# Optimization experiments

Hardware: AMD Instinct MI355X
Metric: run time of the kernel (lower is better)

Reference implementation:

```python
import jax, jax.numpy as jnp
import numpy as np

OUTPUT_SIZES = [1, 3, 6, 8]  # SPP pyramid -> total KV length 110

def _bounds(n, out):
    # PyTorch AdaptiveMaxPool2d bin boundaries
    return [((i * n) // out, -((-(i + 1) * n) // out)) for i in range(out)]

def adaptive_max_pool2d(x, out):
    # x: [B, C, H, W] -> [B, C, out, out]
    B, C, H, W = x.shape
    rows = jnp.stack([x[:, :, s:e, :].max(axis=2) for s, e in _bounds(H, out)], axis=2)
    return jnp.stack([rows[:, :, :, s:e].max(axis=3) for s, e in _bounds(W, out)], axis=3)

def spp(x):
    # [B, C, H, W] -> [B, C, S] with S = sum(o*o) = 110
    B, C = x.shape[:2]
    return jnp.concatenate(
        [adaptive_max_pool2d(x, o).reshape(B, C, o * o) for o in OUTPUT_SIZES], axis=2)

def conv1x1(x, w):
    # 1x1 conv, no bias: w [O, C], x [B, C, H, W]
    return jnp.einsum('oc,bchw->bohw', w, x)

def setup_inputs() -> dict:
    key = jax.random.key(0)
    ks = jax.random.split(key, 6)
    B, C, H, W = 16, 512, 64, 64
    IC = C // 2
    x = jax.random.normal(ks[0], (B, C, H, W), jnp.float32)
    y = jax.random.normal(ks[1], (B, C, H, W), jnp.float32)
    sc = 1.0 / np.sqrt(C)
    w_phi = jax.random.normal(ks[2], (IC, C), jnp.float32) * sc
    w_theta = jax.random.normal(ks[3], (IC, C), jnp.float32) * sc
    w_g = jax.random.normal(ks[4], (IC, C), jnp.float32) * sc
    w_mask = jax.random.normal(ks[5], (C, IC), jnp.float32) * (1.0 / np.sqrt(IC))
    return {"x": x, "y": y, "w_phi": w_phi, "w_theta": w_theta,
            "w_g": w_g, "w_mask": w_mask}

def reference(x, y, w_phi, w_theta, w_g, w_mask):
    B, C, H, W = x.shape
    IC = w_phi.shape[0]
    N = H * W
    # Query: [B, N, IC]
    x_phi = conv1x1(x, w_phi).reshape(B, IC, N).transpose(0, 2, 1)
    # Keys/values from SPP-pooled y: [B, IC, S] / [B, S, IC]
    y_theta = spp(conv1x1(y, w_theta))
    y_g = spp(conv1x1(y, w_g)).transpose(0, 2, 1)
    # Attention with softmax over the QUERY axis (dim=1), as in the source
    attn = jax.nn.softmax(jnp.einsum('bnc,bcs->bns', x_phi, y_theta), axis=1)
    agg = jnp.einsum('bns,bsc->bnc', attn, y_g)          # [B, N, IC]
    agg = agg.transpose(0, 2, 1).reshape(B, IC, H, W)     # [B, IC, H, W]
    mask = conv1x1(agg, w_mask)                           # [B, C, H, W]
    return mask + x
```

## Files before the change

### kernel.cpp

```cpp
#include <hip/hip_runtime.h>

#define DI __device__ __forceinline__

typedef __attribute__((ext_vector_type(8))) __bf16 bf16x8;
typedef __attribute__((ext_vector_type(4))) float f32x4;

DI unsigned short f2bf(float x) {
  union { float f; unsigned u; } v; v.f = x;
  unsigned r = v.u + 0x7fffu + ((v.u >> 16) & 1u);
  return (unsigned short)(r >> 16);
}
DI float bf2f(unsigned short h) {
  union { unsigned u; float f; } v; v.u = ((unsigned)h) << 16;
  return v.f;
}
DI unsigned pack2(float a, float b) {
  return (unsigned)f2bf(a) | (((unsigned)f2bf(b)) << 16);
}

DI void gl_lds16(const void* g, void* l) {
  __builtin_amdgcn_global_load_lds(
      (const __attribute__((address_space(1))) void*)g,
      (__attribute__((address_space(3))) void*)l, 16, 0, 0);
}

__global__ __launch_bounds__(256) void pw_conv(
    const float* __restrict__ w_theta, const float* __restrict__ w_g,
    unsigned short* __restrict__ wTG)
{
  int e = (blockIdx.x * 256 + threadIdx.x) * 8;
  const float* src = (e < 131072) ? (w_theta + e) : (w_g + (e - 131072));
  float4 a = *(const float4*)src;
  float4 c = *(const float4*)(src + 4);
  uint4 u;
  u.x = pack2(a.x, a.y); u.y = pack2(a.z, a.w);
  u.z = pack2(c.x, c.y); u.w = pack2(c.z, c.w);
  *(uint4*)(wTG + e) = u;
}

__constant__ int c_RS[18] = {0, 0,21,42, 0,10,21,32,42,53, 0,8,16,24,32,40,48,56};
__constant__ int c_RE[18] = {64, 22,43,64, 11,22,32,43,54,64, 8,16,24,32,40,48,56,64};

__global__ __launch_bounds__(256) void k1f_conv_pool(
    const float* __restrict__ y, const unsigned short* __restrict__ wTG,
    unsigned short* __restrict__ Rbuf)
{
  const int tid = threadIdx.x;
  const int id = blockIdx.x;
  const int tile = (id & 7) * 16 + (id >> 3);
  const int mb = (tile & 3) * 128;
  const int nbt = tile >> 2;
  const int nb = nbt * 128;
  const int b  = blockIdx.y;
  const int lane = tid & 63, wv = tid >> 6;
  const int wm = (wv & 1) * 64, wn = (wv >> 1) * 64;
  const int l15 = lane & 15, l4 = lane >> 4;

  __shared__ __align__(16) char smem[2 * 18432];
  float* P = (float*)smem;

  const int xn = tid & 127, xh = tid >> 7;
  const float* ycol = y + ((size_t)(b * 512 + xh * 16)) * 4096 + nb + xn;

  f32x4 acc[4][4];
  #pragma unroll
  for (int i = 0; i < 4; ++i)
    #pragma unroll
    for (int j = 0; j < 4; ++j) acc[i][j] = f32x4{0.f, 0.f, 0.f, 0.f};

  float xrA[16], xrB[16];
  auto yload = [&](float* xr, int kb) {
    const float* p = ycol + (size_t)kb * 4096;
    #pragma unroll
    for (int k = 0; k < 16; ++k) xr[k] = p[(size_t)k * 4096];
  };
  auto dmaA = [&](int buf, int kb) {
    unsigned short* As = (unsigned short*)(smem + buf * 18432);
    #pragma unroll
    for (int p = 0; p < 2; ++p) {
      int chunk = (wv * 2 + p) * 64 + lane;
      int row = chunk >> 2, c16 = chunk & 3;
      gl_lds16(wTG + ((size_t)(mb + row)) * 512 + kb + c16 * 8,
               As + (wv * 2 + p) * 512);
    }
  };
  auto bwrite = [&](int buf, const float* xr) {
    unsigned short* Bs = (unsigned short*)(smem + buf * 18432 + 8192);
    unsigned u[8];
    #pragma unroll
    for (int k = 0; k < 16; k += 2) u[k >> 1] = pack2(xr[k], xr[k + 1]);
    uint4* d = (uint4*)&Bs[xn * 40 + xh * 16];
    d[0] = make_uint4(u[0], u[1], u[2], u[3]);
    d[1] = make_uint4(u[4], u[5], u[6], u[7]);
  };
  auto mfma_step = [&](int buf) {
    const unsigned short* As = (const unsigned short*)(smem + buf * 18432);
    const unsigned short* Bs = As + 4096;
    bf16x8 af[4], bfr[4];
    #pragma unroll
    for (int i = 0; i < 4; ++i)
      af[i] = *(const bf16x8*)&As[(wm + i * 16 + l15) * 32 + l4 * 8];
    #pragma unroll
    for (int j = 0; j < 4; ++j)
      bfr[j] = *(const bf16x8*)&Bs[(wn + j * 16 + l15) * 40 + l4 * 8];
    #pragma unroll
    for (int i = 0; i < 4; ++i)
      #pragma unroll
      for (int j = 0; j < 4; ++j)
        acc[i][j] = __builtin_amdgcn_mfma_f32_16x16x32_bf16(af[i], bfr[j], acc[i][j], 0, 0, 0);
  };

  yload(xrA, 0);
  dmaA(0, 0);
  bwrite(0, xrA);
  yload(xrB, 32);
  __syncthreads();
  for (int t = 0; t < 16; t += 2) {
    dmaA(1, (t + 1) * 32);
    bwrite(1, xrB);
    if (t + 2 < 16) yload(xrA, (t + 2) * 32);
    mfma_step(0);
    __syncthreads();
    if (t + 2 < 16) { dmaA(0, (t + 2) * 32); bwrite(0, xrA); }
    if (t + 3 < 16) yload(xrB, (t + 3) * 32);
    mfma_step(1);
    __syncthreads();
  }

  const int hloc = wv >> 1;
  #pragma unroll
  for (int pass = 0; pass < 2; ++pass) {
    __syncthreads();
    if (hloc == pass) {
      #pragma unroll
      for (int i = 0; i < 4; ++i)
        #pragma unroll
        for (int j = 0; j < 4; ++j)
          #pragma unroll
          for (int r = 0; r < 4; ++r)
            P[(wm + i * 16 + l4 * 4 + r) * 65 + j * 16 + l15] = acc[i][j][r];
    }
    __syncthreads();
    const int o = tid & 127;
    size_t rbase = (((size_t)(b * 64 + nbt * 2 + pass)) * 18) * 512 + mb + o;
    if (tid < 128) {
      float b0 = -3.4e38f, b1 = b0, b2 = b0, b3 = b0;
      #pragma unroll
      for (int w = 0; w < 64; ++w) {
        float v = P[o * 65 + w];
        b0 = fmaxf(b0, v);
        if (w < 22) b1 = fmaxf(b1, v);
        if (w >= 21 && w < 43) b2 = fmaxf(b2, v);
        if (w >= 42) b3 = fmaxf(b3, v);
      }
      Rbuf[rbase]           = f2bf(b0);
      Rbuf[rbase + 512]     = f2bf(b1);
      Rbuf[rbase + 2 * 512] = f2bf(b2);
      Rbuf[rbase + 3 * 512] = f2bf(b3);
    } else {
      float s6[6], s8[8];
      #pragma unroll
      for (int i = 0; i < 6; ++i) s6[i] = -3.4e38f;
      #pragma unroll
      for (int i = 0; i < 8; ++i) s8[i] = -3.4e38f;
      constexpr int R6S[6] = {0, 10, 21, 32, 42, 53};
      constexpr int R6E[6] = {11, 22, 32, 43, 54, 64};
      #pragma unroll
      for (int w = 0; w < 64; ++w) {
        float v = P[o * 65 + w];
        #pragma unroll
        for (int i = 0; i < 6; ++i)
          if (w >= R6S[i] && w < R6E[i]) s6[i] = fmaxf(s6[i], v);
        s8[w >> 3] = fmaxf(s8[w >> 3], v);
      }
      #pragma unroll
      for (int i = 0; i < 6; ++i) Rbuf[rbase + (size_t)(4 + i) * 512] = f2bf(s6[i]);
      #pragma unroll
      for (int i = 0; i < 8; ++i) Rbuf[rbase + (size_t)(10 + i) * 512] = f2bf(s8[i]);
    }
  }
}

__global__ __launch_bounds__(256) void k2_pool_final(
    const unsigned short* __restrict__ Rbuf, float* __restrict__ Pt,
    float* __restrict__ Pg)
{
  const int s = blockIdx.x, b = blockIdx.y, tid = threadIdx.x;
  size_t obase = ((size_t)(b * 128) + s) * 256 + tid;
  if (s >= 110) { Pt[obase] = 0.f; Pg[obase] = 0.f; return; }
  int he, wb;
  if (s == 0)      { he = 0; wb = 0; }
  else if (s < 10) { int i = s - 1;  he = 1 + i / 3;  wb = 1 + i % 3; }
  else if (s < 46) { int i = s - 10; he = 4 + i / 6;  wb = 4 + i % 6; }
  else             { int i = s - 46; he = 10 + i / 8; wb = 10 + i % 8; }
  float m0 = -3.4e38f, m1 = -3.4e38f;
  int e = c_RE[he];
  for (int h = c_RS[he]; h < e; ++h) {
    const unsigned short* r = Rbuf + (((size_t)(b * 64 + h)) * 18 + wb) * 512;
    m0 = fmaxf(m0, bf2f(r[tid]));
    m1 = fmaxf(m1, bf2f(r[tid + 256]));
  }
  Pt[obase] = m0;
  Pg[obase] = m1;
}

__global__ __launch_bounds__(256) void k3_fused(
    const float* __restrict__ Pt, const float* __restrict__ Pg,
    const float* __restrict__ w_phi, const float* __restrict__ w_mask,
    unsigned short* __restrict__ Kth, unsigned short* __restrict__ Ktl,
    unsigned short* __restrict__ Vb)
{
  __shared__ __align__(16) char sm3[51200];
  const int tid = threadIdx.x;
  const int tx = tid & 15, ty = tid >> 4;
  const int b = blockIdx.y;
  if (blockIdx.z == 0) {
    const int ct = blockIdx.x;
    const int c0 = tx * 4, s0 = ty * 8;
    float* Ls = (float*)sm3;
    float* Ws = Ls + 128 * 64;
    float acc[8][4] = {};
    for (int kc = 0; kc < 256; kc += 64) {
      #pragma unroll
      for (int j = 0; j < 8; ++j) {
        int flat = tid + 256 * j;
        int row = flat >> 4, k4 = (flat & 15) << 2;
        *(float4*)&Ls[row * 64 + k4] =
            *(const float4*)(Pt + ((size_t)(b * 128) + row) * 256 + kc + k4);
      }
      #pragma unroll
      for (int j = 0; j < 4; ++j) {
        int flat = tid + 256 * j;
        int row = flat >> 4, c4 = (flat & 15) << 2;
        *(float4*)&Ws[row * 68 + c4] =
            *(const float4*)(w_phi + (size_t)(kc + row) * 512 + ct * 64 + c4);
      }
      __syncthreads();
      for (int k = 0; k < 64; k += 4) {
        float4 wv[4];
        #pragma unroll
        for (int kk = 0; kk < 4; ++kk) wv[kk] = *(const float4*)&Ws[(k + kk) * 68 + c0];
        #pragma unroll
        for (int i = 0; i < 8; ++i) {
          float4 a = *(const float4*)&Ls[(s0 + i) * 64 + k];
          const float* ap = (const float*)&a;
          #pragma unroll
          for (int kk = 0; kk < 4; ++kk) {
            const float* wp = (const float*)&wv[kk];
            acc[i][0] += ap[kk] * wp[0];
            acc[i][1] += ap[kk] * wp[1];
            acc[i][2] += ap[kk] * wp[2];
            acc[i][3] += ap[kk] * wp[3];
          }
        }
      }
      __syncthreads();
    }
    #pragma unroll
    for (int i = 0; i < 8; ++i) {
      unsigned short hi[4]; float lo[4];
      #pragma unroll
      for (int j = 0; j < 4; ++j) { hi[j] = f2bf(acc[i][j]); lo[j] = acc[i][j] - bf2f(hi[j]); }
      size_t base = ((size_t)(b * 128) + s0 + i) * 512 + ct * 64 + c0;
      uint2 uh; uh.x = (unsigned)hi[0] | ((unsigned)hi[1] << 16);
      uh.y = (unsigned)hi[2] | ((unsigned)hi[3] << 16);
      uint2 ul; ul.x = pack2(lo[0], lo[1]); ul.y = pack2(lo[2], lo[3]);
      *(uint2*)&Kth[base] = uh;
      *(uint2*)&Ktl[base] = ul;
    }
  } else {
    const int ot = blockIdx.x;
    const int o0 = ty * 4;
    float* Ws = (float*)sm3;
    float* Ps = Ws + 64 * 64;
    float acc[4][8] = {};
    for (int kc = 0; kc < 256; kc += 64) {
      #pragma unroll
      for (int j = 0; j < 4; ++j) {
        int flat = tid + 256 * j;
        int row = flat >> 4, k4 = (flat & 15) << 2;
        *(float4*)&Ws[row * 64 + k4] =
            *(const float4*)(w_mask + (size_t)(ot * 64 + row) * 256 + kc + k4);
      }
      #pragma unroll
      for (int j = 0; j < 8; ++j) {
        int flat = tid + 256 * j;
        int row = flat >> 4, k4 = (flat & 15) << 2;
        *(float4*)&Ps[row * 68 + k4] =
            *(const float4*)(Pg + ((size_t)(b * 128) + row) * 256 + kc + k4);
      }
      __syncthreads();
      for (int k = 0; k < 64; k += 4) {
        float4 wv[4];
        #pragma unroll
        for (int i = 0; i < 4; ++i) wv[i] = *(const float4*)&Ws[(o0 + i) * 64 + k];
        #pragma unroll
        for (int jj = 0; jj < 8; ++jj) {
          float4 pv = *(const float4*)&Ps[(tx + 16 * jj) * 68 + k];
          const float* pp = (const float*)&pv;
          #pragma unroll
          for (int i = 0; i < 4; ++i) {
            const float* wp = (const float*)&wv[i];
            #pragma unroll
            for (int kk = 0; kk < 4; ++kk) acc[i][jj] += wp[kk] * pp[kk];
          }
        }
      }
      __syncthreads();
    }
    #pragma unroll
    for (int i = 0; i < 4; ++i)
      #pragma unroll
      for (int jj = 0; jj < 8; ++jj)
        Vb[((size_t)(b * 512) + ot * 64 + o0 + i) * 128 + tx + 16 * jj] =
            f2bf(acc[i][jj]);
  }
}

__global__ __launch_bounds__(256) void k4_scores(
    const float* __restrict__ x, const unsigned short* __restrict__ Kth,
    const unsigned short* __restrict__ Ktl, float* __restrict__ scoresT,
    float* __restrict__ pmax_g, float* __restrict__ psum_g)
{
  const int tid = threadIdx.x;
  const int ntile = blockIdx.x;
  const int nb = ntile * 128;
  const int b = blockIdx.y;
  const int lane = tid & 63, wv = tid >> 6;
  const int wm = (wv & 1) * 64, wn = (wv >> 1) * 64;
  const int l15 = lane & 15, l4 = lane >> 4;
  __shared__ __align__(16) char smem4[2 * 26624];
  __shared__ float SmP[256], SsP[256];

  const int xn = tid & 127, xh = tid >> 7;
  const float* xcol = x + ((size_t)(b * 512 + xh * 16)) * 4096 + nb + xn;

  f32x4 acc[4][4];
  #pragma unroll
  for (int i = 0; i < 4; ++i)
    #pragma unroll
    for (int j = 0; j < 4; ++j) acc[i][j] = f32x4{0.f, 0.f, 0.f, 0.f};

  float xrA[16], xrB[16];
  auto xload = [&](float* xr, int kb) {
    const float* p = xcol + (size_t)kb * 4096;
    #pragma unroll
    for (int k = 0; k < 16; ++k) xr[k] = p[(size_t)k * 4096];
  };
  auto dmaA = [&](int buf, int kb) {
    unsigned short* Ah = (unsigned short*)(smem4 + buf * 26624);
    unsigned short* Al = Ah + 4096;
    #pragma unroll
    for (int p = 0; p < 2; ++p) {
      int chunk = (wv * 2 + p) * 64 + lane;
      int row = chunk >> 2, c16 = chunk & 3;
      size_t g = ((size_t)(b * 128) + row) * 512 + kb + c16 * 8;
      gl_lds16(Kth + g, Ah + (wv * 2 + p) * 512);
      gl_lds16(Ktl + g, Al + (wv * 2 + p) * 512);
    }
  };
  auto bwrite = [&](int buf, const float* xr) {
    unsigned short* Bs = (unsigned short*)(smem4 + buf * 26624 + 16384);
    unsigned u[8];
    #pragma unroll
    for (int k = 0; k < 16; k += 2) u[k >> 1] = pack2(xr[k], xr[k + 1]);
    uint4* d = (uint4*)&Bs[xn * 40 + xh * 16];
    d[0] = make_uint4(u[0], u[1], u[2], u[3]);
    d[1] = make_uint4(u[4], u[5], u[6], u[7]);
  };
  auto mfma_step = [&](int buf) {
    const unsigned short* Ah = (const unsigned short*)(smem4 + buf * 26624);
    const unsigned short* Al = Ah + 4096;
    const unsigned short* Bs = Al + 4096;
    bf16x8 ah[4], al[4], bfr[4];
    #pragma unroll
    for (int i = 0; i < 4; ++i) {
      ah[i] = *(const bf16x8*)&Ah[(wm + i * 16 + l15) * 32 + l4 * 8];
      al[i] = *(const bf16x8*)&Al[(wm + i * 16 + l15) * 32 + l4 * 8];
    }
    #pragma unroll
    for (int j = 0; j < 4; ++j)
      bfr[j] = *(const bf16x8*)&Bs[(wn + j * 16 + l15) * 40 + l4 * 8];
    #pragma unroll
    for (int i = 0; i < 4; ++i)
      #pragma unroll
      for (int j = 0; j < 4; ++j) {
        acc[i][j] = __builtin_amdgcn_mfma_f32_16x16x32_bf16(ah[i], bfr[j], acc[i][j], 0, 0, 0);
        acc[i][j] = __builtin_amdgcn_mfma_f32_16x16x32_bf16(al[i], bfr[j], acc[i][j], 0, 0, 0);
      }
  };

  xload(xrA, 0);
  dmaA(0, 0);
  bwrite(0, xrA);
  xload(xrB, 32);
  __syncthreads();
  for (int t = 0; t < 16; t += 2) {
    dmaA(1, (t + 1) * 32);
    bwrite(1, xrB);
    if (t + 2 < 16) xload(xrA, (t + 2) * 32);
    mfma_step(0);
    __syncthreads();
    if (t + 2 < 16) { dmaA(0, (t + 2) * 32); bwrite(0, xrA); }
    if (t + 3 < 16) xload(xrB, (t + 3) * 32);
    mfma_step(1);
    __syncthreads();
  }

  #pragma unroll
  for (int i = 0; i < 4; ++i)
    #pragma unroll
    for (int j = 0; j < 4; ++j)
      *(float4*)(scoresT + ((size_t)(b * 4096) + nb + wn + j * 16 + l15) * 128 +
                 wm + i * 16 + l4 * 4) = *(float4*)&acc[i][j];

  const int nh = wn >> 6;
  float cm[4][4];
  #pragma unroll
  for (int i = 0; i < 4; ++i)
    #pragma unroll
    for (int r = 0; r < 4; ++r) {
      float v = fmaxf(fmaxf(acc[i][0][r], acc[i][1][r]),
                      fmaxf(acc[i][2][r], acc[i][3][r]));
      v = fmaxf(v, __shfl_xor(v, 1));
      v = fmaxf(v, __shfl_xor(v, 2));
      v = fmaxf(v, __shfl_xor(v, 4));
      v = fmaxf(v, __shfl_xor(v, 8));
      if (l15 == 0) SmP[(wm + i * 16 + l4 * 4 + r) * 2 + nh] = v;
    }
  __syncthreads();
  #pragma unroll
  for (int i = 0; i < 4; ++i)
    #pragma unroll
    for (int r = 0; r < 4; ++r) {
      int s = wm + i * 16 + l4 * 4 + r;
      cm[i][r] = fmaxf(SmP[s * 2], SmP[s * 2 + 1]);
    }
  #pragma unroll
  for (int i = 0; i < 4; ++i)
    #pragma unroll
    for (int r = 0; r < 4; ++r) {
      float s0 = __expf(acc[i][0][r] - cm[i][r]) + __expf(acc[i][1][r] - cm[i][r]) +
                 __expf(acc[i][2][r] - cm[i][r]) + __expf(acc[i][3][r] - cm[i][r]);
      s0 += __shfl_xor(s0, 1);
      s0 += __shfl_xor(s0, 2);
      s0 += __shfl_xor(s0, 4);
      s0 += __shfl_xor(s0, 8);
      if (l15 == 0) SsP[(wm + i * 16 + l4 * 4 + r) * 2 + nh] = s0;
    }
  __syncthreads();
  if (tid < 128) {
    size_t pidx = ((size_t)(b * 128) + tid) * 32 + ntile;
    pmax_g[pidx] = fmaxf(SmP[tid * 2], SmP[tid * 2 + 1]);
    psum_g[pidx] = SsP[tid * 2] + SsP[tid * 2 + 1];
  }
}

__global__ __launch_bounds__(256) void k5e_exp(
    const float* __restrict__ scoresT, const float* __restrict__ pmax_g,
    const float* __restrict__ psum_g, unsigned short* __restrict__ Eb)
{
  const int b = blockIdx.y, tid = threadIdx.x;
  __shared__ float sm[128], sl[128];
  if (tid < 128) {
    float M = 0.f, linv = 0.f;
    if (tid < 110) {
      const float* pm = pmax_g + ((size_t)(b * 128) + tid) * 32;
      const float* ps = psum_g + ((size_t)(b * 128) + tid) * 32;
      M = -3.4e38f;
      #pragma unroll
      for (int t = 0; t < 32; ++t) M = fmaxf(M, pm[t]);
      float S = 0.f;
      #pragma unroll
      for (int t = 0; t < 32; ++t) S += ps[t] * __expf(pm[t] - M);
      linv = 1.f / S;
    }
    sm[tid] = M; sl[tid] = linv;
  }
  __syncthreads();
  const size_t base = (size_t)b * 4096 * 128;
  #pragma unroll
  for (int j = 0; j < 8; ++j) {
    int chunk = blockIdx.x * 2048 + j * 256 + tid;
    int sc = (chunk & 31) * 4;
    float4 v = *(const float4*)(scoresT + base + (size_t)chunk * 4);
    float e0 = __expf(v.x - sm[sc])     * sl[sc];
    float e1 = __expf(v.y - sm[sc + 1]) * sl[sc + 1];
    float e2 = __expf(v.z - sm[sc + 2]) * sl[sc + 2];
    float e3 = __expf(v.w - sm[sc + 3]) * sl[sc + 3];
    uint2 u; u.x = pack2(e0, e1); u.y = pack2(e2, e3);
    *(uint2*)(Eb + base + (size_t)chunk * 4) = u;
  }
}

__global__ __launch_bounds__(256) void k6_out(
    const unsigned short* __restrict__ Eb, const unsigned short* __restrict__ Vb,
    const float* __restrict__ x, float* __restrict__ out)
{
  const int tid = threadIdx.x;
  const int id = blockIdx.x;
  const int tile = (id & 7) * 16 + (id >> 3);
  const int mb = (tile & 3) * 128;
  const int nb = (tile >> 2) * 128;
  const int b = blockIdx.y;
  const int lane = tid & 63, wv = tid >> 6;
  const int wm = (wv & 1) * 64, wn = (wv >> 1) * 64;
  const int l15 = lane & 15, l4 = lane >> 4;
  __shared__ __align__(16) unsigned short SA[4][4096];
  __shared__ __align__(16) unsigned short SB[4][4096];

  #pragma unroll
  for (int h = 0; h < 4; ++h)
    #pragma unroll
    for (int p = 0; p < 2; ++p) {
      int chunk = (wv * 2 + p) * 64 + lane;
      int row = chunk >> 2, c16 = chunk & 3;
      gl_lds16(Vb + ((size_t)(b * 512) + mb + row) * 128 + h * 32 + c16 * 8,
               &SA[h][(wv * 2 + p) * 512]);
      gl_lds16(Eb + ((size_t)(b * 4096) + nb + row) * 128 + h * 32 + c16 * 8,
               &SB[h][(wv * 2 + p) * 512]);
    }

  float xr[4][4][4];
  #pragma unroll
  for (int i = 0; i < 4; ++i)
    #pragma unroll
    for (int j = 0; j < 4; ++j)
      #pragma unroll
      for (int r = 0; r < 4; ++r)
        xr[i][j][r] = x[((size_t)(b * 512) + mb + wm + i * 16 + l4 * 4 + r) * 4096 +
                        nb + wn + j * 16 + l15];

  f32x4 acc[4][4];
  #pragma unroll
  for (int i = 0; i < 4; ++i)
    #pragma unroll
    for (int j = 0; j < 4; ++j) acc[i][j] = f32x4{0.f, 0.f, 0.f, 0.f};

  __syncthreads();
  #pragma unroll
  for (int h = 0; h < 4; ++h) {
    bf16x8 af[4], bfr[4];
    #pragma unroll
    for (int i = 0; i < 4; ++i)
      af[i] = *(const bf16x8*)&SA[h][(wm + i * 16 + l15) * 32 + l4 * 8];
    #pragma unroll
    for (int j = 0; j < 4; ++j)
      bfr[j] = *(const bf16x8*)&SB[h][(wn + j * 16 + l15) * 32 + l4 * 8];
    #pragma unroll
    for (int i = 0; i < 4; ++i)
      #pragma unroll
      for (int j = 0; j < 4; ++j)
        acc[i][j] = __builtin_amdgcn_mfma_f32_16x16x32_bf16(af[i], bfr[j], acc[i][j], 0, 0, 0);
  }
  #pragma unroll
  for (int i = 0; i < 4; ++i)
    #pragma unroll
    for (int j = 0; j < 4; ++j)
      #pragma unroll
      for (int r = 0; r < 4; ++r) {
        int o = mb + wm + i * 16 + l4 * 4 + r;
        size_t idx = ((size_t)(b * 512) + o) * 4096 + nb + wn + j * 16 + l15;
        out[idx] = acc[i][j][r] + xr[i][j][r];
      }
}

extern "C" void kernel_launch(void* const* d_in, const int* in_sizes, int n_in,
                              void* d_out, int out_size, void* d_ws, size_t ws_size,
                              hipStream_t stream)
{
  (void)in_sizes; (void)n_in; (void)out_size; (void)ws_size;
  const float* x       = (const float*)d_in[0];
  const float* y       = (const float*)d_in[1];
  const float* w_phi   = (const float*)d_in[2];
  const float* w_theta = (const float*)d_in[3];
  const float* w_g     = (const float*)d_in[4];
  const float* w_mask  = (const float*)d_in[5];
  float* out = (float*)d_out;

  char* ws = (char*)d_ws;
  char* B0 = ws + 67108864;
  unsigned short* Rbuf = (unsigned short*)B0;
  float* scoresT = (float*)B0;
  unsigned short* Eb = (unsigned short*)(B0 + 33554432);
  unsigned short* wTG = (unsigned short*)(B0 + 50331648);
  unsigned short* Vb  = (unsigned short*)(B0 + 50331648);
  float* pmax_g = (float*)(B0 + 52428800);
  float* psum_g = (float*)(B0 + 52690944);
  char* C0 = B0 + 54525952;
  float* Pt = (float*)C0;
  float* Pg = (float*)(C0 + 2097152);
  unsigned short* Kth = (unsigned short*)(C0 + 4194304);
  unsigned short* Ktl = (unsigned short*)(C0 + 6291456);

  pw_conv<<<dim3(128), 256, 0, stream>>>(w_theta, w_g, wTG);
  k1f_conv_pool<<<dim3(128, 16), 256, 0, stream>>>(y, wTG, Rbuf);
  k2_pool_final<<<dim3(128, 16), 256, 0, stream>>>(Rbuf, Pt, Pg);
  k3_fused<<<dim3(8, 16, 2), 256, 0, stream>>>(Pt, Pg, w_phi, w_mask, Kth, Ktl, Vb);
  k4_scores<<<dim3(32, 16), 256, 0, stream>>>(x, Kth, Ktl, scoresT, pmax_g, psum_g);
  k5e_exp<<<dim3(64, 16), 256, 0, stream>>>(scoresT, pmax_g, psum_g, Eb);
  k6_out<<<dim3(128, 16), 256, 0, stream>>>(Eb, Vb, x, out);
}
```

Baseline: 487.4 us.

## Triple-buffer GEMM mainloops with explicit vmcnt waits and vectorized activation loads

In the conv+pool and scores kernels, the main loops move from a double-buffered schedule with two __syncthreads per pair of steps to a triple-buffered LDS ring. Each step now has a single s_barrier gated by hand-counted s_waitcnt vmcnt values, so async DMA and activation loads stay in flight across MFMA steps. Activation loads switch from 16 scalar strided loads per thread to four float4 loads, each thread now covering 4 positions by 4 channels. The B-tile LDS writes are reshaped to match. This raises LDS use, which may lower occupancy, and the hardcoded vmcnt counts are fragile if the compiler reorders or splits memory operations.

```diff
diff --git a/kernel.cpp b/kernel.cpp
--- a/kernel.cpp
+++ b/kernel.cpp
@@ -23,6 +23,12 @@
       (const __attribute__((address_space(1))) void*)g,
       (__attribute__((address_space(3))) void*)l, 16, 0, 0);
 }
+
+DI void wt_vm0()  { asm volatile("s_waitcnt vmcnt(0) lgkmcnt(0)" ::: "memory"); }
+DI void wt_vm6()  { asm volatile("s_waitcnt vmcnt(6) lgkmcnt(0)" ::: "memory"); }
+DI void wt_vm8()  { asm volatile("s_waitcnt vmcnt(8) lgkmcnt(0)" ::: "memory"); }
+DI void wt_vm10() { asm volatile("s_waitcnt vmcnt(10) lgkmcnt(0)" ::: "memory"); }
+DI void wt_vm12() { asm volatile("s_waitcnt vmcnt(12) lgkmcnt(0)" ::: "memory"); }
 
 __global__ __launch_bounds__(256) void pw_conv(
     const float* __restrict__ w_theta, const float* __restrict__ w_g,
@@ -56,11 +62,11 @@
   const int wm = (wv & 1) * 64, wn = (wv >> 1) * 64;
   const int l15 = lane & 15, l4 = lane >> 4;
 
-  __shared__ __align__(16) char smem[2 * 18432];
+  __shared__ __align__(16) char smem[3 * 18432];
   float* P = (float*)smem;
 
-  const int xn = tid & 127, xh = tid >> 7;
-  const float* ycol = y + ((size_t)(b * 512 + xh * 16)) * 4096 + nb + xn;
+  const int c4 = tid & 7, n4 = tid >> 3;
+  const float* ycol = y + ((size_t)(b * 512)) * 4096 + nb + n4 * 4;
 
   f32x4 acc[4][4];
   #pragma unroll
@@ -68,30 +74,32 @@
     #pragma unroll
     for (int j = 0; j < 4; ++j) acc[i][j] = f32x4{0.f, 0.f, 0.f, 0.f};
 
-  float xrA[16], xrB[16];
+  float xr0[16], xr1[16];
   auto yload = [&](float* xr, int kb) {
-    const float* p = ycol + (size_t)kb * 4096;
-    #pragma unroll
-    for (int k = 0; k < 16; ++k) xr[k] = p[(size_t)k * 4096];
+    #pragma unroll
+    for (int cc = 0; cc < 4; ++cc)
+      *(float4*)&xr[cc * 4] =
+          *(const float4*)(ycol + (size_t)(kb + c4 * 4 + cc) * 4096);
   };
   auto dmaA = [&](int buf, int kb) {
     unsigned short* As = (unsigned short*)(smem + buf * 18432);
     #pragma unroll
     for (int p = 0; p < 2; ++p) {
       int chunk = (wv * 2 + p) * 64 + lane;
-      int row = chunk >> 2, c16 = chunk & 3;
-      gl_lds16(wTG + ((size_t)(mb + row)) * 512 + kb + c16 * 8,
+      int row = chunk >> 2, cc16 = chunk & 3;
+      gl_lds16(wTG + ((size_t)(mb + row)) * 512 + kb + cc16 * 8,
                As + (wv * 2 + p) * 512);
     }
   };
   auto bwrite = [&](int buf, const float* xr) {
     unsigned short* Bs = (unsigned short*)(smem + buf * 18432 + 8192);
-    unsigned u[8];
-    #pragma unroll
-    for (int k = 0; k < 16; k += 2) u[k >> 1] = pack2(xr[k], xr[k + 1]);
-    uint4* d = (uint4*)&Bs[xn * 40 + xh * 16];
-    d[0] = make_uint4(u[0], u[1], u[2], u[3]);
-    d[1] = make_uint4(u[4], u[5], u[6], u[7]);
+    #pragma unroll
+    for (int q = 0; q < 4; ++q) {
+      uint2 u;
+      u.x = pack2(xr[q], xr[4 + q]);
+      u.y = pack2(xr[8 + q], xr[12 + q]);
+      *(uint2*)&Bs[(n4 * 4 + q) * 40 + c4 * 4] = u;
+    }
   };
   auto mfma_step = [&](int buf) {
     const unsigned short* As = (const unsigned short*)(smem + buf * 18432);
@@ -110,21 +118,21 @@
         acc[i][j] = __builtin_amdgcn_mfma_f32_16x16x32_bf16(af[i], bfr[j], acc[i][j], 0, 0, 0);
   };
 
-  yload(xrA, 0);
+  yload(xr0, 0);
   dmaA(0, 0);
-  bwrite(0, xrA);
-  yload(xrB, 32);
-  __syncthreads();
-  for (int t = 0; t < 16; t += 2) {
-    dmaA(1, (t + 1) * 32);
-    bwrite(1, xrB);
-    if (t + 2 < 16) yload(xrA, (t + 2) * 32);
-    mfma_step(0);
-    __syncthreads();
-    if (t + 2 < 16) { dmaA(0, (t + 2) * 32); bwrite(0, xrA); }
-    if (t + 3 < 16) yload(xrB, (t + 3) * 32);
-    mfma_step(1);
-    __syncthreads();
+  bwrite(0, xr0);
+  yload(xr1, 32);
+  #pragma unroll
+  for (int t = 0; t < 16; ++t) {
+    if (t + 1 < 16) dmaA((t + 1) % 3, (t + 1) * 32);
+    if (t + 2 < 16) yload((t & 1) ? xr1 : xr0, (t + 2) * 32);
+    if (t < 14) wt_vm10();
+    else if (t == 14) wt_vm6();
+    else wt_vm0();
+    __builtin_amdgcn_s_barrier();
+    __builtin_amdgcn_sched_barrier(0);
+    mfma_step(t % 3);
+    if (t + 1 < 16) bwrite((t + 1) % 3, (t & 1) ? xr0 : xr1);
   }
 
   const int hloc = wv >> 1;
@@ -231,9 +239,9 @@
       #pragma unroll
       for (int j = 0; j < 4; ++j) {
         int flat = tid + 256 * j;
-        int row = flat >> 4, c4 = (flat & 15) << 2;
-        *(float4*)&Ws[row * 68 + c4] =
-            *(const float4*)(w_phi + (size_t)(kc + row) * 512 + ct * 64 + c4);
+        int row = flat >> 4, cc4 = (flat & 15) << 2;
+        *(float4*)&Ws[row * 68 + cc4] =
+            *(const float4*)(w_phi + (size_t)(kc + row) * 512 + ct * 64 + cc4);
       }
       __syncthreads();
       for (int k = 0; k < 64; k += 4) {
@@ -329,11 +337,11 @@
   const int lane = tid & 63, wv = tid >> 6;
   const int wm = (wv & 1) * 64, wn = (wv >> 1) * 64;
   const int l15 = lane & 15, l4 = lane >> 4;
-  __shared__ __align__(16) char smem4[2 * 26624];
+  __shared__ __align__(16) char smem4[3 * 26624];
   __shared__ float SmP[256], SsP[256];
 
-  const int xn = tid & 127, xh = tid >> 7;
-  const float* xcol = x + ((size_t)(b * 512 + xh * 16)) * 4096 + nb + xn;
+  const int c4 = tid & 7, n4 = tid >> 3;
+  const float* xcol = x + ((size_t)(b * 512)) * 4096 + nb + n4 * 4;
 
   f32x4 acc[4][4];
   #pragma unroll
@@ -341,11 +349,12 @@
     #pragma unroll
     for (int j = 0; j < 4; ++j) acc[i][j] = f32x4{0.f, 0.f, 0.f, 0.f};
 
-  float xrA[16], xrB[16];
+  float xr0[16], xr1[16];
   auto xload = [&](float* xr, int kb) {
-    const float* p = xcol + (size_t)kb * 4096;
-    #pragma unroll
-    for (int k = 0; k < 16; ++k) xr[k] = p[(size_t)k * 4096];
+    #pragma unroll
+    for (int cc = 0; cc < 4; ++cc)
+      *(float4*)&xr[cc * 4] =
+          *(const float4*)(xcol + (size_t)(kb + c4 * 4 + cc) * 4096);
   };
   auto dmaA = [&](int buf, int kb) {
     unsigned short* Ah = (unsigned short*)(smem4 + buf * 26624);
@@ -353,20 +362,21 @@
     #pragma unroll
     for (int p = 0; p < 2; ++p) {
       int chunk = (wv * 2 + p) * 64 + lane;
-      int row = chunk >> 2, c16 = chunk & 3;
-      size_t g = ((size_t)(b * 128) + row) * 512 + kb + c16 * 8;
+      int row = chunk >> 2, cc16 = chunk & 3;
+      size_t g = ((size_t)(b * 128) + row) * 512 + kb + cc16 * 8;
       gl_lds16(Kth + g, Ah + (wv * 2 + p) * 512);
       gl_lds16(Ktl + g, Al + (wv * 2 + p) * 512);
     }
   };
   auto bwrite = [&](int buf, const float* xr) {
     unsigned short* Bs = (unsigned short*)(smem4 + buf * 26624 + 16384);
-    unsigned u[8];
-    #pragma unroll
-    for (int k = 0; k < 16; k += 2) u[k >> 1] = pack2(xr[k], xr[k + 1]);
-    uint4* d = (uint4*)&Bs[xn * 40 + xh * 16];
-    d[0] = make_uint4(u[0], u[1], u[2], u[3]);
-    d[1] = make_uint4(u[4], u[5], u[6], u[7]);
+    #pragma unroll
+    for (int q = 0; q < 4; ++q) {
+      uint2 u;
+      u.x = pack2(xr[q], xr[4 + q]);
+      u.y = pack2(xr[8 + q], xr[12 + q]);
+      *(uint2*)&Bs[(n4 * 4 + q) * 40 + c4 * 4] = u;
+    }
   };
   auto mfma_step = [&](int buf) {
     const unsigned short* Ah = (const unsigned short*)(smem4 + buf * 26624);
@@ -390,21 +400,21 @@
       }
   };
 
-  xload(xrA, 0);
+  xload(xr0, 0);
   dmaA(0, 0);
-  bwrite(0, xrA);
-  xload(xrB, 32);
-  __syncthreads();
-  for (int t = 0; t < 16; t += 2) {
-    dmaA(1, (t + 1) * 32);
-    bwrite(1, xrB);
-    if (t + 2 < 16) xload(xrA, (t + 2) * 32);
-    mfma_step(0);
-    __syncthreads();
-    if (t + 2 < 16) { dmaA(0, (t + 2) * 32); bwrite(0, xrA); }
-    if (t + 3 < 16) xload(xrB, (t + 3) * 32);
-    mfma_step(1);
-    __syncthreads();
+  bwrite(0, xr0);
+  xload(xr1, 32);
+  #pragma unroll
+  for (int t = 0; t < 16; ++t) {
+    if (t + 1 < 16) dmaA((t + 1) % 3, (t + 1) * 32);
+    if (t + 2 < 16) xload((t & 1) ? xr1 : xr0, (t + 2) * 32);
+    if (t < 14) wt_vm12();
+    else if (t == 14) wt_vm8();
+    else wt_vm0();
+    __builtin_amdgcn_s_barrier();
+    __builtin_amdgcn_sched_barrier(0);
+    mfma_step(t % 3);
+    if (t + 1 < 16) bwrite((t + 1) % 3, (t & 1) ? xr0 : xr1);
   }
 
   #pragma unroll
```

Result: no change. 493.2 us (+1.2%).
